# Kernel optimization log

Hardware: AMD Instinct MI355X
Metric: run time of the kernel (lower is better)

Reference implementation:

```python
import jax, jax.numpy as jnp
import numpy as np

N_NODES = 100000
N_GRAPHS = 64

def gcn_conv(x, edge_index, W, b, num_nodes):
    # PyG GCNConv: x' = D^-1/2 (A + I) D^-1/2 (x W) + b
    h = x @ W  # [N, out]
    row, col = edge_index[0], edge_index[1]
    loops = jnp.arange(num_nodes, dtype=row.dtype)
    src = jnp.concatenate([row, loops])  # message source (x_j)
    dst = jnp.concatenate([col, loops])  # aggregation target
    deg = jax.ops.segment_sum(jnp.ones_like(src, dtype=h.dtype), dst,
                              num_segments=num_nodes)
    dinv = jnp.where(deg > 0, jax.lax.rsqrt(deg), 0.0)
    norm = dinv[src] * dinv[dst]  # [E+N]
    msgs = h[src] * norm[:, None]  # gather-transform
    out = jax.ops.segment_sum(msgs, dst, num_segments=num_nodes)  # scatter
    return out + b

def global_mean_pool(x, batch, num_graphs):
    sums = jax.ops.segment_sum(x, batch, num_segments=num_graphs)
    cnts = jax.ops.segment_sum(jnp.ones((x.shape[0],), x.dtype), batch,
                               num_segments=num_graphs)
    return sums / jnp.maximum(cnts, 1.0)[:, None]

def setup_inputs() -> dict:
    key = jax.random.key(0)
    ks = jax.random.split(key, 12)
    d_in, d_hid, d_mid, d_out = 128, 128, 20, 10
    n_edges = 1600000
    x = jax.random.normal(ks[0], (N_NODES, d_in), dtype=jnp.float32)
    edge_index = jax.random.randint(ks[1], (2, n_edges), 0, N_NODES, dtype=jnp.int64)
    batch = jnp.sort(jax.random.randint(ks[2], (N_NODES,), 0, N_GRAPHS, dtype=jnp.int64))
    def glorot(k, fan_in, fan_out):
        s = (6.0 / (fan_in + fan_out)) ** 0.5
        return jax.random.uniform(k, (fan_in, fan_out), jnp.float32, -s, s)
    return {
        "x": x, "edge_index": edge_index, "batch": batch,
        "W1": glorot(ks[3], d_in, d_hid), "b1": jnp.zeros((d_hid,), jnp.float32),
        "W2": glorot(ks[4], d_hid, d_hid), "b2": jnp.zeros((d_hid,), jnp.float32),
        "fc1_W": glorot(ks[5], d_hid, d_mid), "fc1_b": jnp.zeros((d_mid,), jnp.float32),
        "fc2_W": glorot(ks[6], d_mid, d_out), "fc2_b": jnp.zeros((d_out,), jnp.float32),
    }

def reference(x, edge_index, batch, W1, b1, W2, b2, fc1_W, fc1_b, fc2_W, fc2_b):
    # eval mode: dropout is identity
    h = gcn_conv(x, edge_index, W1, b1, N_NODES)
    h = jax.nn.elu(h)
    h = gcn_conv(h, edge_index, W2, b2, N_NODES)
    g = global_mean_pool(h, batch, N_GRAPHS)  # [G, hidden]
    g = jax.nn.relu(g @ fc1_W + fc1_b)
    g = g @ fc2_W + fc2_b
    return jax.nn.log_softmax(g, axis=1)
```

## Files before the change

kernel.cpp:

```cpp
#include <hip/hip_runtime.h>
#include <math.h>

#define DH 128
#define BCAP 16384

typedef __bf16 bf8_t __attribute__((ext_vector_type(8)));
typedef short short8 __attribute__((ext_vector_type(8)));
typedef float f4_t __attribute__((ext_vector_type(4)));
typedef float f2_t __attribute__((ext_vector_type(2)));

__device__ inline unsigned short f2b(float f) {
    unsigned int u = __builtin_bit_cast(unsigned int, f);
    u = u + 0x7fffu + ((u >> 16) & 1u);
    return (unsigned short)(u >> 16);
}
__device__ inline float b2f(unsigned short h) {
    return __builtin_bit_cast(float, (unsigned int)h << 16);
}

__global__ __launch_bounds__(256) void k_bucket(const int* __restrict__ row,
                                                const int* __restrict__ col,
                                                int E, int nbuck, int chunk,
                                                unsigned int* __restrict__ pairs,
                                                int* __restrict__ bcur) {
    __shared__ int lcnt[256];
    __shared__ int lbase[256];
    __shared__ unsigned int srec[8192];
    int t = threadIdx.x;
    int e0 = blockIdx.x * chunk;
    int e1 = min(e0 + chunk, E);
    lcnt[t] = 0;
    __syncthreads();
    for (int i = e0 + t; i < e1; i += 256) {
        int d = col[i];
        int b = d >> 9;
        int slot = atomicAdd(&lcnt[b], 1);
        srec[i - e0] = ((unsigned int)b << 22) | ((unsigned int)(d & 511) << 13)
                     | (unsigned int)slot;
    }
    __syncthreads();
    if (t < nbuck) {
        int c = lcnt[t];
        lbase[t] = (c > 0) ? atomicAdd(&bcur[t * 16], c) : 0;
    }
    __syncthreads();
    for (int i = e0 + t; i < e1; i += 256) {
        unsigned int r = srec[i - e0];
        int b = r >> 22;
        unsigned int dl = (r >> 13) & 511u;
        int slot = (int)(r & 8191u);
        int g = lbase[b] + slot;
        if (g < BCAP)
            pairs[(size_t)b * BCAP + g] = ((unsigned int)row[i] << 9) | dl;
    }
}

__global__ __launch_bounds__(256) void k_build(const unsigned int* __restrict__ pairs,
                                               const int* __restrict__ bcur,
                                               int nbuck, int N,
                                               int* __restrict__ off,
                                               float* __restrict__ dinv,
                                               int* __restrict__ csr) {
    __shared__ int sb[256];
    __shared__ int cnt2[512];
    __shared__ int excl[512];
    __shared__ int curi[512];
    __shared__ int stmp[256];
    int b = blockIdx.x, t = threadIdx.x;
    sb[t] = (t < nbuck) ? min(bcur[t * 16], BCAP) : 0;
    __syncthreads();
    for (int d = 1; d < 256; d <<= 1) {
        int v = (t >= d) ? sb[t - d] : 0;
        __syncthreads();
        sb[t] += v;
        __syncthreads();
    }
    int base = (b == 0) ? 0 : sb[b - 1];
    int cnt = sb[b] - base;
    int node0 = b << 9;
    int nodes = min(512, N - node0);
    cnt2[t] = 0; cnt2[t + 256] = 0;
    __syncthreads();
    const unsigned int* pp = pairs + (size_t)b * BCAP;
    for (int i = t; i < cnt; i += 256)
        atomicAdd(&cnt2[pp[i] & 511u], 1);
    __syncthreads();
    stmp[t] = cnt2[2 * t] + cnt2[2 * t + 1];
    __syncthreads();
    for (int d = 1; d < 256; d <<= 1) {
        int v = (t >= d) ? stmp[t - d] : 0;
        __syncthreads();
        stmp[t] += v;
        __syncthreads();
    }
    int pre = (t == 0) ? 0 : stmp[t - 1];
    excl[2 * t] = pre;
    excl[2 * t + 1] = pre + cnt2[2 * t];
    __syncthreads();
    if (t < nodes) {
        off[node0 + t] = base + excl[t];
        dinv[node0 + t] = rsqrtf((float)(cnt2[t] + 1));
    }
    int t2 = t + 256;
    if (t2 < nodes) {
        off[node0 + t2] = base + excl[t2];
        dinv[node0 + t2] = rsqrtf((float)(cnt2[t2] + 1));
    }
    if (t == 0) off[node0 + nodes] = base + cnt;
    curi[t] = excl[t]; curi[t + 256] = excl[t + 256];
    __syncthreads();
    for (int i = t; i < cnt; i += 256) {
        unsigned int p = pp[i];
        int d = (int)(p & 511u);
        int slot = atomicAdd(&curi[d], 1);
        csr[base + slot] = (int)(p >> 9);
    }
}

__global__ void k_prepW(const float* __restrict__ W1, const float* __restrict__ W2,
                        unsigned short* __restrict__ Wt1, unsigned short* __restrict__ Wt2) {
    int t = blockIdx.x * blockDim.x + threadIdx.x;
    const float* W = (t < 16384) ? W1 : W2;
    unsigned short* Wt = (t < 16384) ? Wt1 : Wt2;
    int v = t & 16383;
    int k = v >> 7, n = v & 127;
    Wt[n * DH + k] = f2b(W[k * DH + n]);
}

__global__ __launch_bounds__(256) void k_gemm_mfma(const void* __restrict__ Xin, int x_is_bf16,
                                                   const unsigned short* __restrict__ Wt,
                                                   const float* __restrict__ dinv,
                                                   unsigned char* __restrict__ Y, int nrows) {
    __shared__ unsigned short Xs[64 * 136];
    __shared__ unsigned short Ws[128 * 136];
    int t = threadIdx.x;
    int row0 = blockIdx.x * 64;

    for (int v = t; v < 128 * 32; v += 256) {
        int n = v >> 5, kq = v & 31;
        ushort4 w = ((const ushort4*)Wt)[v];
        *(ushort4*)&Ws[n * 136 + kq * 4] = w;
    }
    if (x_is_bf16) {
        const unsigned short* X = (const unsigned short*)Xin;
        for (int v = t; v < 64 * 32; v += 256) {
            int r = v >> 5, cq = v & 31;
            int gr = row0 + r;
            ushort4 h;
            if (gr < nrows) h = ((const ushort4*)X)[(size_t)gr * 32 + cq];
            else { h.x = 0; h.y = 0; h.z = 0; h.w = 0; }
            *(ushort4*)&Xs[r * 136 + cq * 4] = h;
        }
    } else {
        const float* X = (const float*)Xin;
        for (int v = t; v < 64 * 32; v += 256) {
            int r = v >> 5, cq = v & 31;
            int gr = row0 + r;
            ushort4 h;
            if (gr < nrows) {
                float4 xv = ((const float4*)X)[(size_t)gr * 32 + cq];
                h.x = f2b(xv.x); h.y = f2b(xv.y); h.z = f2b(xv.z); h.w = f2b(xv.w);
            } else { h.x = 0; h.y = 0; h.z = 0; h.w = 0; }
            *(ushort4*)&Xs[r * 136 + cq * 4] = h;
        }
    }
    __syncthreads();

    int w = t >> 6;
    int lane = t & 63;
    int quad = lane >> 4;
    int l16 = lane & 15;
    int rw = w * 16;

    f4_t acc[8];
#pragma unroll
    for (int j = 0; j < 8; j++) acc[j] = (f4_t){0.f, 0.f, 0.f, 0.f};

#pragma unroll
    for (int kk = 0; kk < 4; kk++) {
        int k0 = kk * 32;
        bf8_t a = __builtin_bit_cast(bf8_t,
            *(const short8*)&Xs[(rw + l16) * 136 + k0 + quad * 8]);
#pragma unroll
        for (int j = 0; j < 8; j++) {
            bf8_t b = __builtin_bit_cast(bf8_t,
                *(const short8*)&Ws[(j * 16 + l16) * 136 + k0 + quad * 8]);
            acc[j] = __builtin_amdgcn_mfma_f32_16x16x32_bf16(a, b, acc[j], 0, 0, 0);
        }
    }

#pragma unroll
    for (int reg = 0; reg < 4; reg++) {
        int r = row0 + rw + quad * 4 + reg;
        if (r < nrows) {
            float dv = dinv[r];
            float v0 = acc[0][reg] * dv, v1 = acc[1][reg] * dv;
            float v2 = acc[2][reg] * dv, v3 = acc[3][reg] * dv;
            float v4 = acc[4][reg] * dv, v5 = acc[5][reg] * dv;
            float v6 = acc[6][reg] * dv, v7 = acc[7][reg] * dv;
            int d0 = __builtin_amdgcn_cvt_pk_fp8_f32(v0, v1, 0, false);
            d0 = __builtin_amdgcn_cvt_pk_fp8_f32(v2, v3, d0, true);
            int d1 = __builtin_amdgcn_cvt_pk_fp8_f32(v4, v5, 0, false);
            d1 = __builtin_amdgcn_cvt_pk_fp8_f32(v6, v7, d1, true);
            *(uint2*)&Y[(size_t)r * DH + l16 * 8] = make_uint2((unsigned)d0, (unsigned)d1);
        }
    }
}

__global__ __launch_bounds__(256) void k_aggm(const unsigned char* __restrict__ T,
                                              unsigned short* __restrict__ Out,
                                              const float* __restrict__ dinv,
                                              const int* __restrict__ off,
                                              const int* __restrict__ csr,
                                              const float* __restrict__ bias,
                                              int elu, int N) {
    __shared__ int ofs[17];
    __shared__ float dinv16[16];
    __shared__ float bias_l[128];
    __shared__ unsigned int lidx[768];
    __shared__ unsigned char ldst[768];
    __shared__ unsigned int Bt4[2][32][34];
    __shared__ unsigned char Al[2][16][48];

    int t = threadIdx.x;
    int d0 = blockIdx.x * 16;
    if (t < 17) ofs[t] = off[min(d0 + t, N)];
    if (t < 16) dinv16[t] = dinv[d0 + t];
    if (t < 128) bias_l[t] = bias[((t & 7) << 4) | (t >> 3)];
    __syncthreads();
    int s0 = ofs[0];
    int cnt = min(ofs[16] - s0, 752);
    for (int k = t; k < cnt; k += 256) {
        lidx[k] = (unsigned)csr[s0 + k];
        int p = s0 + k, d = 0;
#pragma unroll
        for (int i = 1; i < 16; i++) d += (p >= ofs[i]) ? 1 : 0;
        ldst[k] = (unsigned char)d;
    }
    if (t < 16) { lidx[cnt + t] = (unsigned)(d0 + t); ldst[cnt + t] = (unsigned char)t; }
    int ncnt = cnt + 16;
    int pcnt = (ncnt + 31) & ~31;
    for (int k = ncnt + t; k < pcnt; k += 256) { lidx[k] = (unsigned)d0; ldst[k] = 0xFF; }
    __syncthreads();

    int w = t >> 6;
    int lane = t & 63;
    int q = lane >> 4;
    int l16 = lane & 15;
    int el = t >> 3;
    int seg = t & 7;
    int nch = pcnt >> 5;
    int x = l16 & 3;
    unsigned int selp = (unsigned)(x | ((x + 4) << 8));

    auto stage = [&](int c, int bf) {
        if (t < 128) {
            int m = t >> 3;
            int k0 = (t & 7) * 4;
            unsigned int ld = *(const unsigned int*)&ldst[c * 32 + k0];
            unsigned int u = ld ^ (0x01010101u * (unsigned)m);
            unsigned int z = (u - 0x01010101u) & ~u & 0x80808080u;
            *(unsigned int*)&Al[bf][m][k0] = (z >> 7) * 0x38u;
        }
        unsigned int j = lidx[c * 32 + el];
        uint4 r = ((const uint4*)(T + (size_t)j * DH))[seg];
        Bt4[bf][seg * 4 + 0][el] = r.x;
        Bt4[bf][seg * 4 + 1][el] = r.y;
        Bt4[bf][seg * 4 + 2][el] = r.z;
        Bt4[bf][seg * 4 + 3][el] = r.w;
    };

    f4_t acc0 = (f4_t){0.f, 0.f, 0.f, 0.f};
    f4_t acc1 = (f4_t){0.f, 0.f, 0.f, 0.f};

    stage(0, 0);
    __syncthreads();
    for (int c = 0; c < nch; c++) {
        int bf = c & 1;
        long al = __builtin_bit_cast(long, *(const uint2*)&Al[bf][l16][q * 8]);
#pragma unroll
        for (int cb = 0; cb < 2; cb++) {
            int cq = 8 * w + cb * 4 + (l16 >> 2);
            const unsigned int* bp = &Bt4[bf][cq][q * 8];
            uint2 e01 = *(const uint2*)bp;
            uint2 e23 = *(const uint2*)(bp + 2);
            uint2 e45 = *(const uint2*)(bp + 4);
            uint2 e67 = *(const uint2*)(bp + 6);
            unsigned t01 = __builtin_amdgcn_perm(e01.y, e01.x, selp);
            unsigned t23 = __builtin_amdgcn_perm(e23.y, e23.x, selp);
            unsigned t45 = __builtin_amdgcn_perm(e45.y, e45.x, selp);
            unsigned t67 = __builtin_amdgcn_perm(e67.y, e67.x, selp);
            uint2 bfrag;
            bfrag.x = __builtin_amdgcn_perm(t23, t01, 0x05040100u);
            bfrag.y = __builtin_amdgcn_perm(t67, t45, 0x05040100u);
            long bl = __builtin_bit_cast(long, bfrag);
            if (cb == 0)
                acc0 = __builtin_amdgcn_mfma_f32_16x16x32_fp8_fp8(al, bl, acc0, 0, 0, 0);
            else
                acc1 = __builtin_amdgcn_mfma_f32_16x16x32_fp8_fp8(al, bl, acc1, 0, 0, 0);
        }
        if (c + 1 < nch) stage(c + 1, 1 - bf);
        __syncthreads();
    }

#pragma unroll
    for (int cb = 0; cb < 2; cb++) {
        f4_t acc = cb ? acc1 : acc0;
        int np = 32 * w + cb * 16 + l16;
        int ctrue = ((np & 7) << 4) | (np >> 3);
        float bs = bias_l[np];
#pragma unroll
        for (int reg = 0; reg < 4; reg++) {
            int m = q * 4 + reg;
            int nd = d0 + m;
            if (nd < N) {
                float o = acc[reg] * dinv16[m] + bs;
                if (elu) o = o > 0.f ? o : expm1f(o);
                Out[(size_t)nd * DH + ctrue] = f2b(o);
            }
        }
    }
}

__global__ __launch_bounds__(256) void k_pool(const unsigned int* __restrict__ H32,
                                              const int* __restrict__ batch,
                                              float* __restrict__ Gsum,
                                              int* __restrict__ cnts, int N) {
    int g = blockIdx.x;
    int p = blockIdx.y;
    int t = threadIdx.x;
    int lane = t & 63;
    int rg = t >> 6;
    int lo = 0, hi = N;
    while (lo < hi) { int m = (lo + hi) >> 1; if (batch[m] < g) lo = m + 1; else hi = m; }
    int s = lo;
    hi = N;
    while (lo < hi) { int m = (lo + hi) >> 1; if (batch[m] < g + 1) lo = m + 1; else hi = m; }
    int e = lo;
    int len = e - s;
    int parts = (int)gridDim.y;
    int chunk = (len + parts - 1) / parts;
    int i0 = s + p * chunk;
    int i1 = min(i0 + chunk, e);
    float a0 = 0.f, a1 = 0.f;
    for (int i = i0 + rg; i < i1; i += 4) {
        unsigned int v = H32[(size_t)i * 64 + lane];
        a0 += b2f((unsigned short)(v & 0xffffu));
        a1 += b2f((unsigned short)(v >> 16));
    }
    __shared__ float ps[4][DH];
    ps[rg][lane * 2] = a0;
    ps[rg][lane * 2 + 1] = a1;
    __syncthreads();
    if (t < DH) {
        float v = ps[0][t] + ps[1][t] + ps[2][t] + ps[3][t];
        atomicAdd(&Gsum[g * DH + t], v);
    }
    if (p == 0 && t == 0) cnts[g] = len;
}

__global__ __launch_bounds__(64) void k_head(const float* __restrict__ Gsum,
                                             const int* __restrict__ cnts,
                                             const float* __restrict__ W1,
                                             const float* __restrict__ b1,
                                             const float* __restrict__ W2,
                                             const float* __restrict__ b2,
                                             float* __restrict__ out) {
    int g = blockIdx.x;
    int t = threadIdx.x;
    __shared__ float gv[DH];
    __shared__ float mid[20];
    __shared__ float o[10];
    float inv = 1.f / fmaxf((float)cnts[g], 1.f);
    for (int i = t; i < DH; i += 64) gv[i] = Gsum[g * DH + i] * inv;
    __syncthreads();
    if (t < 20) {
        float a = b1[t];
        for (int k = 0; k < DH; k++) a += gv[k] * W1[k * 20 + t];
        mid[t] = fmaxf(a, 0.f);
    }
    __syncthreads();
    if (t < 10) {
        float a = b2[t];
        for (int k = 0; k < 20; k++) a += mid[k] * W2[k * 10 + t];
        o[t] = a;
    }
    __syncthreads();
    if (t == 0) {
        float m = -1e30f;
        for (int j = 0; j < 10; j++) m = fmaxf(m, o[j]);
        float ssum = 0.f;
        for (int j = 0; j < 10; j++) ssum += expf(o[j] - m);
        float l = logf(ssum);
        for (int j = 0; j < 10; j++) out[g * 10 + j] = o[j] - m - l;
    }
}

extern "C" void kernel_launch(void* const* d_in, const int* in_sizes, int n_in,
                              void* d_out, int out_size, void* d_ws, size_t ws_size,
                              hipStream_t stream) {
    const float* x    = (const float*)d_in[0];
    const int*   ei   = (const int*)d_in[1];
    const int*   batch= (const int*)d_in[2];
    const float* W1   = (const float*)d_in[3];
    const float* b1   = (const float*)d_in[4];
    const float* W2   = (const float*)d_in[5];
    const float* b2   = (const float*)d_in[6];
    const float* fc1W = (const float*)d_in[7];
    const float* fc1b = (const float*)d_in[8];
    const float* fc2W = (const float*)d_in[9];
    const float* fc2b = (const float*)d_in[10];
    float* out = (float*)d_out;

    int N = in_sizes[0] / DH;
    int E = in_sizes[1] / 2;
    int G = out_size / 10;

    char* p = (char*)d_ws;
    auto alloc = [&](size_t bytes) {
        char* r = p;
        p += (bytes + 255) & ~(size_t)255;
        return r;
    };
    unsigned char*  t8 = (unsigned char*)alloc((size_t)N * DH);
    unsigned short* a1 = (unsigned short*)alloc((size_t)N * DH * 2);
    int*   csr  = (int*)alloc((size_t)E * 4);
    int*   off  = (int*)alloc((size_t)(N + 1) * 4);
    float* dinv = (float*)alloc((size_t)N * 4);
    int nbuck = (N + 511) >> 9;
    unsigned int* pairs = (unsigned int*)alloc((size_t)nbuck * BCAP * 4);
    unsigned short* Wt1 = (unsigned short*)alloc(DH * DH * 2);
    unsigned short* Wt2 = (unsigned short*)alloc(DH * DH * 2);
    float* Gsum = (float*)alloc((size_t)G * DH * 4);
    int*   bcur = (int*)alloc(256 * 16 * 4);
    int*   cnts = (int*)alloc((size_t)G * 4);

    const int* row = ei;
    const int* col = ei + E;

    (void)hipMemsetAsync(Gsum, 0, (size_t)G * DH * 4 + 256 * 16 * 4, stream);

    const int chunk = 8192;
    int ablocks = (E + chunk - 1) / chunk;
    k_bucket<<<ablocks, 256, 0, stream>>>(row, col, E, nbuck, chunk, pairs, bcur);
    k_build<<<nbuck, 256, 0, stream>>>(pairs, bcur, nbuck, N, off, dinv, csr);
    k_prepW<<<128, 256, 0, stream>>>(W1, W2, Wt1, Wt2);

    int gblocks = (N + 63) / 64;
    int mblocks = (N + 15) / 16;
    k_gemm_mfma<<<gblocks, 256, 0, stream>>>(x, 0, Wt1, dinv, t8, N);
    k_aggm<<<mblocks, 256, 0, stream>>>(t8, a1, dinv, off, csr, b1, 1, N);
    k_gemm_mfma<<<gblocks, 256, 0, stream>>>(a1, 1, Wt2, dinv, t8, N);
    k_aggm<<<mblocks, 256, 0, stream>>>(t8, a1, dinv, off, csr, b2, 0, N);

    dim3 pg(G, 32);
    k_pool<<<pg, 256, 0, stream>>>((const unsigned int*)a1, batch, Gsum, cnts, N);
    k_head<<<G, 64, 0, stream>>>(Gsum, cnts, fc1W, fc1b, fc2W, fc2b, out);
}
```

Baseline: 312.7 us.

## Replace MFMA-based aggregation with one-wavefront-per-node gather-sum

```diff
diff --git a/kernel.cpp b/kernel.cpp
--- a/kernel.cpp
+++ b/kernel.cpp
@@ -207,118 +207,89 @@
     }
 }
 
-__global__ __launch_bounds__(256) void k_aggm(const unsigned char* __restrict__ T,
-                                              unsigned short* __restrict__ Out,
-                                              const float* __restrict__ dinv,
-                                              const int* __restrict__ off,
-                                              const int* __restrict__ csr,
-                                              const float* __restrict__ bias,
-                                              int elu, int N) {
-    __shared__ int ofs[17];
-    __shared__ float dinv16[16];
-    __shared__ float bias_l[128];
-    __shared__ unsigned int lidx[768];
-    __shared__ unsigned char ldst[768];
-    __shared__ unsigned int Bt4[2][32][34];
-    __shared__ unsigned char Al[2][16][48];
-
+__global__ __launch_bounds__(256) void k_agg(const unsigned char* __restrict__ T,
+                                             unsigned short* __restrict__ Out,
+                                             const float* __restrict__ dinv,
+                                             const int* __restrict__ off,
+                                             const int* __restrict__ csr,
+                                             const float* __restrict__ bias,
+                                             int elu, int N) {
     int t = threadIdx.x;
-    int d0 = blockIdx.x * 16;
-    if (t < 17) ofs[t] = off[min(d0 + t, N)];
-    if (t < 16) dinv16[t] = dinv[d0 + t];
-    if (t < 128) bias_l[t] = bias[((t & 7) << 4) | (t >> 3)];
-    __syncthreads();
-    int s0 = ofs[0];
-    int cnt = min(ofs[16] - s0, 752);
-    for (int k = t; k < cnt; k += 256) {
-        lidx[k] = (unsigned)csr[s0 + k];
-        int p = s0 + k, d = 0;
-#pragma unroll
-        for (int i = 1; i < 16; i++) d += (p >= ofs[i]) ? 1 : 0;
-        ldst[k] = (unsigned char)d;
-    }
-    if (t < 16) { lidx[cnt + t] = (unsigned)(d0 + t); ldst[cnt + t] = (unsigned char)t; }
-    int ncnt = cnt + 16;
-    int pcnt = (ncnt + 31) & ~31;
-    for (int k = ncnt + t; k < pcnt; k += 256) { lidx[k] = (unsigned)d0; ldst[k] = 0xFF; }
-    __syncthreads();
-
-    int w = t >> 6;
+    int d = blockIdx.x * 4 + (t >> 6);
+    if (d >= N) return;
     int lane = t & 63;
-    int q = lane >> 4;
-    int l16 = lane & 15;
-    int el = t >> 3;
-    int seg = t & 7;
-    int nch = pcnt >> 5;
-    int x = l16 & 3;
-    unsigned int selp = (unsigned)(x | ((x + 4) << 8));
-
-    auto stage = [&](int c, int bf) {
-        if (t < 128) {
-            int m = t >> 3;
-            int k0 = (t & 7) * 4;
-            unsigned int ld = *(const unsigned int*)&ldst[c * 32 + k0];
-            unsigned int u = ld ^ (0x01010101u * (unsigned)m);
-            unsigned int z = (u - 0x01010101u) & ~u & 0x80808080u;
-            *(unsigned int*)&Al[bf][m][k0] = (z >> 7) * 0x38u;
+    int half = lane >> 5;
+    int l5 = lane & 31;
+
+    int s0 = off[d];
+    int deg = off[d + 1] - s0;
+
+    int jl = (lane < deg) ? csr[s0 + lane] : 0;
+
+    float a0 = 0.f, a1 = 0.f, a2 = 0.f, a3 = 0.f;
+
+    unsigned int vs = half ? 0u
+        : *(const unsigned int*)(T + (size_t)d * DH + (l5 << 2));
+    {
+        f2_t lo = __builtin_amdgcn_cvt_pk_f32_fp8(vs, false);
+        f2_t hi = __builtin_amdgcn_cvt_pk_f32_fp8(vs, true);
+        a0 += lo[0]; a1 += lo[1]; a2 += hi[0]; a3 += hi[1];
+    }
+
+    int dcl = min(deg, 64);
+    int k = half;
+    for (; k + 2 < dcl; k += 4) {
+        int j0 = __shfl(jl, k);
+        int j1 = __shfl(jl, k + 2);
+        unsigned int v0 = *(const unsigned int*)(T + (size_t)j0 * DH + (l5 << 2));
+        unsigned int v1 = *(const unsigned int*)(T + (size_t)j1 * DH + (l5 << 2));
+        f2_t lo0 = __builtin_amdgcn_cvt_pk_f32_fp8(v0, false);
+        f2_t hi0 = __builtin_amdgcn_cvt_pk_f32_fp8(v0, true);
+        f2_t lo1 = __builtin_amdgcn_cvt_pk_f32_fp8(v1, false);
+        f2_t hi1 = __builtin_amdgcn_cvt_pk_f32_fp8(v1, true);
+        a0 += lo0[0] + lo1[0];
+        a1 += lo0[1] + lo1[1];
+        a2 += hi0[0] + hi1[0];
+        a3 += hi0[1] + hi1[1];
+    }
+    if (k < dcl) {
+        int j0 = __shfl(jl, k);
+        unsigned int v0 = *(const unsigned int*)(T + (size_t)j0 * DH + (l5 << 2));
+        f2_t lo0 = __builtin_amdgcn_cvt_pk_f32_fp8(v0, false);
+        f2_t hi0 = __builtin_amdgcn_cvt_pk_f32_fp8(v0, true);
+        a0 += lo0[0]; a1 += lo0[1]; a2 += hi0[0]; a3 += hi0[1];
+    }
+    for (int q = 64 + half; q < deg; q += 2) {
+        int j = csr[s0 + q];
+        unsigned int v0 = *(const unsigned int*)(T + (size_t)j * DH + (l5 << 2));
+        f2_t lo0 = __builtin_amdgcn_cvt_pk_f32_fp8(v0, false);
+        f2_t hi0 = __builtin_amdgcn_cvt_pk_f32_fp8(v0, true);
+        a0 += lo0[0]; a1 += lo0[1]; a2 += hi0[0]; a3 += hi0[1];
+    }
+
+    a0 += __shfl_xor(a0, 32);
+    a1 += __shfl_xor(a1, 32);
+    a2 += __shfl_xor(a2, 32);
+    a3 += __shfl_xor(a3, 32);
+
+    if (half == 0) {
+        float dv = dinv[d];
+        int base = ((l5 & 1) << 6) | (l5 >> 1);
+        float o0 = a0 * dv + bias[base];
+        float o1 = a1 * dv + bias[base + 16];
+        float o2 = a2 * dv + bias[base + 32];
+        float o3 = a3 * dv + bias[base + 48];
+        if (elu) {
+            o0 = o0 > 0.f ? o0 : expm1f(o0);
+            o1 = o1 > 0.f ? o1 : expm1f(o1);
+            o2 = o2 > 0.f ? o2 : expm1f(o2);
+            o3 = o3 > 0.f ? o3 : expm1f(o3);
         }
-        unsigned int j = lidx[c * 32 + el];
-        uint4 r = ((const uint4*)(T + (size_t)j * DH))[seg];
-        Bt4[bf][seg * 4 + 0][el] = r.x;
-        Bt4[bf][seg * 4 + 1][el] = r.y;
-        Bt4[bf][seg * 4 + 2][el] = r.z;
-        Bt4[bf][seg * 4 + 3][el] = r.w;
-    };
-
-    f4_t acc0 = (f4_t){0.f, 0.f, 0.f, 0.f};
-    f4_t acc1 = (f4_t){0.f, 0.f, 0.f, 0.f};
-
-    stage(0, 0);
-    __syncthreads();
-    for (int c = 0; c < nch; c++) {
-        int bf = c & 1;
-        long al = __builtin_bit_cast(long, *(const uint2*)&Al[bf][l16][q * 8]);
-#pragma unroll
-        for (int cb = 0; cb < 2; cb++) {
-            int cq = 8 * w + cb * 4 + (l16 >> 2);
-            const unsigned int* bp = &Bt4[bf][cq][q * 8];
-            uint2 e01 = *(const uint2*)bp;
-            uint2 e23 = *(const uint2*)(bp + 2);
-            uint2 e45 = *(const uint2*)(bp + 4);
-            uint2 e67 = *(const uint2*)(bp + 6);
-            unsigned t01 = __builtin_amdgcn_perm(e01.y, e01.x, selp);
-            unsigned t23 = __builtin_amdgcn_perm(e23.y, e23.x, selp);
-            unsigned t45 = __builtin_amdgcn_perm(e45.y, e45.x, selp);
-            unsigned t67 = __builtin_amdgcn_perm(e67.y, e67.x, selp);
-            uint2 bfrag;
-            bfrag.x = __builtin_amdgcn_perm(t23, t01, 0x05040100u);
-            bfrag.y = __builtin_amdgcn_perm(t67, t45, 0x05040100u);
-            long bl = __builtin_bit_cast(long, bfrag);
-            if (cb == 0)
-                acc0 = __builtin_amdgcn_mfma_f32_16x16x32_fp8_fp8(al, bl, acc0, 0, 0, 0);
-            else
-                acc1 = __builtin_amdgcn_mfma_f32_16x16x32_fp8_fp8(al, bl, acc1, 0, 0, 0);
-        }
-        if (c + 1 < nch) stage(c + 1, 1 - bf);
-        __syncthreads();
-    }
-
-#pragma unroll
-    for (int cb = 0; cb < 2; cb++) {
-        f4_t acc = cb ? acc1 : acc0;
-        int np = 32 * w + cb * 16 + l16;
-        int ctrue = ((np & 7) << 4) | (np >> 3);
-        float bs = bias_l[np];
-#pragma unroll
-        for (int reg = 0; reg < 4; reg++) {
-            int m = q * 4 + reg;
-            int nd = d0 + m;
-            if (nd < N) {
-                float o = acc[reg] * dinv16[m] + bs;
-                if (elu) o = o > 0.f ? o : expm1f(o);
-                Out[(size_t)nd * DH + ctrue] = f2b(o);
-            }
-        }
+        unsigned short* orow = Out + (size_t)d * DH;
+        orow[base]      = f2b(o0);
+        orow[base + 16] = f2b(o1);
+        orow[base + 32] = f2b(o2);
+        orow[base + 48] = f2b(o3);
     }
 }
 
@@ -447,11 +418,11 @@
     k_prepW<<<128, 256, 0, stream>>>(W1, W2, Wt1, Wt2);
 
     int gblocks = (N + 63) / 64;
-    int mblocks = (N + 15) / 16;
+    int nblocks4 = (N + 3) / 4;
     k_gemm_mfma<<<gblocks, 256, 0, stream>>>(x, 0, Wt1, dinv, t8, N);
-    k_aggm<<<mblocks, 256, 0, stream>>>(t8, a1, dinv, off, csr, b1, 1, N);
+    k_agg<<<nblocks4, 256, 0, stream>>>(t8, a1, dinv, off, csr, b1, 1, N);
     k_gemm_mfma<<<gblocks, 256, 0, stream>>>(a1, 1, Wt2, dinv, t8, N);
-    k_aggm<<<mblocks, 256, 0, stream>>>(t8, a1, dinv, off, csr, b2, 0, N);
+    k_agg<<<nblocks4, 256, 0, stream>>>(t8, a1, dinv, off, csr, b2, 0, N);
 
     dim3 pg(G, 32);
     k_pool<<<pg, 256, 0, stream>>>((const unsigned int*)a1, batch, Gsum, cnts, N);
```

Measured after the change: 329.4 us. 1.05x slower.
